# Performance work log

Hardware: AMD Instinct MI355X
Metric: run time of the kernel (lower is better)

## Reference

```python
import jax, jax.numpy as jnp
import numpy as np

V, N, H = 4, 4096, 128
EDGE_P = 0.002  # sparsity of generated adjacency


def setup_inputs() -> dict:
    key = jax.random.key(0)
    ks = jax.random.split(key, 12)
    # binary adjacency, zero diagonal (dense_to_sparse treats nonzeros as edges)
    adjs = (jax.random.uniform(ks[0], (V, N, N)) < EDGE_P).astype(jnp.float32)
    idx = jnp.arange(N)
    adjs = adjs.at[:, idx, idx].set(0.0)
    s = 0.05
    return {
        "adjs": adjs,
        "w1": jax.random.normal(ks[1], (V, N, H), jnp.float32) * s,
        "b1": jnp.zeros((V, H), jnp.float32),
        "w2": jax.random.normal(ks[2], (V, H, H), jnp.float32) * s,
        "b2": jnp.zeros((V, H), jnp.float32),
        "wa1": jax.random.normal(ks[3], (H, 64), jnp.float32) * s,
        "ba1": jnp.zeros((64,), jnp.float32),
        "wa2": jax.random.normal(ks[4], (64,), jnp.float32) * s,
        "ba2": jnp.zeros((1,), jnp.float32),
        "wf1": jax.random.normal(ks[5], (V * H, 2 * H), jnp.float32) * s,
        "bf1": jnp.zeros((2 * H,), jnp.float32),
        "wf2": jax.random.normal(ks[6], (2 * H, 128), jnp.float32) * s,
        "bf2": jnp.zeros((128,), jnp.float32),
    }


def _gcn_norm(adjs):
    # GCNConv default: A_hat = A + I, A_norm = D^-1/2 A_hat D^-1/2 (edge weight 1)
    n = adjs.shape[-1]
    idx = jnp.arange(n)
    a_hat = (adjs != 0).astype(adjs.dtype).at[:, idx, idx].set(1.0)
    dinv = jax.lax.rsqrt(a_hat.sum(-1))  # [V,N], deg>=1 due to self loops
    return dinv[:, :, None] * a_hat * dinv[:, None, :]


def reference(adjs, w1, b1, w2, b2, wa1, ba1, wa2, ba2, wf1, bf1, wf2, bf2):
    a_norm = _gcn_norm(adjs)  # [V,N,N]
    # initial features X = I_N, so X @ w1 == w1; dropout is inference no-op
    h1 = jax.nn.relu(jnp.einsum('vij,vjh->vih', a_norm, w1) + b1[:, None, :])
    h2 = jax.nn.relu(
        jnp.einsum('vij,vjh->vih', a_norm, jnp.einsum('vnh,vhk->vnk', h1, w2))
        + b2[:, None, :])  # [V,N,H] per-view embeddings
    # attention fusion
    summaries = h2.mean(axis=1)  # [V,H]
    scores = jnp.tanh(summaries @ wa1 + ba1) @ wa2 + ba2[0]  # [V]
    attn = jax.nn.softmax(scores, axis=0)  # [V]
    weighted = h2 * attn[:, None, None]  # [V,N,H]
    fusion_in = jnp.transpose(weighted, (1, 0, 2)).reshape(weighted.shape[1], -1)  # [N, V*H]
    fused = jax.nn.relu(fusion_in @ wf1 + bf1) @ wf2 + bf2  # [N, fusion_out]
    return fused, attn, h2
```

## Files before the change

kernel.cpp:

```cpp
#include <hip/hip_runtime.h>

#define VV 4
#define NN 4096
#define HH 128
#define CAP 64
#define GR 32
#define FR 8
#define CHP (NN / GR)

typedef __attribute__((ext_vector_type(4))) float fvec4;

__global__ __launch_bounds__(256) void k_build_csr(
    const float* __restrict__ adjs, int* __restrict__ nbr,
    int* __restrict__ cnt, float* __restrict__ dinv)
{
    int wave = threadIdx.x >> 6;
    int lane = threadIdx.x & 63;
    int r = blockIdx.x * 4 + wave;
    const fvec4* row = (const fvec4*)(adjs + (size_t)r * NN);
    int* out = nbr + (size_t)r * CAP;
    unsigned long long lm = (1ull << lane) - 1ull;
    int base = 0;
    #pragma unroll 4
    for (int c = 0; c < NN / 256; ++c) {
        fvec4 x = __builtin_nontemporal_load(&row[c * 64 + lane]);
        int c0 = (x.x != 0.f), c1 = (x.y != 0.f), c2 = (x.z != 0.f), c3 = (x.w != 0.f);
        unsigned long long b0 = __ballot(c0), b1 = __ballot(c1);
        unsigned long long b2 = __ballot(c2), b3 = __ballot(c3);
        int pos = base + __popcll(b0 & lm) + __popcll(b1 & lm)
                       + __popcll(b2 & lm) + __popcll(b3 & lm);
        int e = c * 256 + lane * 4;
        if (c0 && pos < CAP) out[pos] = e;     pos += c0;
        if (c1 && pos < CAP) out[pos] = e + 1; pos += c1;
        if (c2 && pos < CAP) out[pos] = e + 2; pos += c2;
        if (c3 && pos < CAP) out[pos] = e + 3; pos += c3;
        base += __popcll(b0) + __popcll(b1) + __popcll(b2) + __popcll(b3);
    }
    if (lane == 0) {
        cnt[r]  = base < CAP ? base : CAP;
        dinv[r] = rsqrtf((float)(base + 1));
    }
}

__global__ __launch_bounds__(512) void k_spmm1(
    const float* __restrict__ w1, const float* __restrict__ b1,
    const int* __restrict__ nbr, const int* __restrict__ cnt,
    const float* __restrict__ dinv, float* __restrict__ h1)
{
    int xcd  = blockIdx.x & 7;
    int slot = blockIdx.x >> 3;
    int wid  = (xcd >> 1) * 1024 + slot * 2 + (xcd & 1);
    int g = threadIdx.x >> 7;
    int h = threadIdx.x & 127;
    int r = wid * 4 + g;
    int v = r >> 12;
    __shared__ int   s_j[4][CAP];
    __shared__ float s_w[4][CAP];
    int n = cnt[r];
    float dr = dinv[r];
    if (h < n) {
        int j = nbr[(size_t)r * CAP + h];
        s_j[g][h] = j;
        s_w[g][h] = dinv[v * NN + j];
    }
    __syncthreads();
    float acc = dr * w1[(size_t)r * HH + h];
    #pragma unroll 4
    for (int k = 0; k < n; ++k)
        acc += s_w[g][k] * w1[((size_t)(v * NN + s_j[g][k])) * HH + h];
    float val = dr * acc + b1[v * HH + h];
    h1[(size_t)r * HH + h] = val > 0.f ? val : 0.f;
}

__global__ __launch_bounds__(512) void k_gather2(
    const float* __restrict__ h1, const int* __restrict__ nbr,
    const int* __restrict__ cnt, const float* __restrict__ dinv,
    float* __restrict__ u)
{
    int xcd  = blockIdx.x & 7;
    int slot = blockIdx.x >> 3;
    int wid  = (xcd >> 1) * 1024 + slot * 2 + (xcd & 1);
    int g = threadIdx.x >> 7;
    int h = threadIdx.x & 127;
    int r = wid * 4 + g;
    int v = r >> 12;
    __shared__ int   s_j[4][CAP];
    __shared__ float s_w[4][CAP];
    int n = cnt[r];
    float dr = dinv[r];
    if (h < n) {
        int j = nbr[(size_t)r * CAP + h];
        s_j[g][h] = j;
        s_w[g][h] = dinv[v * NN + j];
    }
    __syncthreads();
    float acc = dr * h1[(size_t)r * HH + h];
    #pragma unroll 4
    for (int k = 0; k < n; ++k)
        acc += s_w[g][k] * h1[((size_t)(v * NN + s_j[g][k])) * HH + h];
    u[(size_t)r * HH + h] = dr * acc;
}

__global__ __launch_bounds__(256) void k_gemm2c(
    const float* __restrict__ u, const float* __restrict__ w2,
    const float* __restrict__ b2, float* __restrict__ h2,
    float* __restrict__ part)
{
    const int bpv = NN / GR;
    int v = blockIdx.x / bpv;
    int rbase_g = blockIdx.x * GR;
    __shared__ float s_u[GR][HH];
    __shared__ float s_p[8][HH];
    const float4* src = (const float4*)(u + (size_t)rbase_g * HH);
    for (int idx = threadIdx.x; idx < GR * HH / 4; idx += 256)
        ((float4*)s_u)[idx] = src[idx];
    __syncthreads();

    int r0 = (threadIdx.x >> 5) * 4;
    int c0 = (threadIdx.x & 31) * 4;
    const float* wv = w2 + (size_t)v * HH * HH;
    float acc[4][4];
    #pragma unroll
    for (int i = 0; i < 4; ++i)
        #pragma unroll
        for (int j = 0; j < 4; ++j) acc[i][j] = 0.f;
    for (int k = 0; k < HH; k += 4) {
        float4 a[4], w[4];
        #pragma unroll
        for (int i = 0; i < 4; ++i) a[i] = *(const float4*)&s_u[r0 + i][k];
        #pragma unroll
        for (int kk = 0; kk < 4; ++kk) w[kk] = *(const float4*)&wv[(size_t)(k + kk) * HH + c0];
        #pragma unroll
        for (int i = 0; i < 4; ++i)
            #pragma unroll
            for (int j = 0; j < 4; ++j) {
                acc[i][j] += a[i].x * ((const float*)&w[0])[j];
                acc[i][j] += a[i].y * ((const float*)&w[1])[j];
                acc[i][j] += a[i].z * ((const float*)&w[2])[j];
                acc[i][j] += a[i].w * ((const float*)&w[3])[j];
            }
    }
    float p[4];
    #pragma unroll
    for (int j = 0; j < 4; ++j) {
        float b = b2[v * HH + c0 + j];
        float s = 0.f;
        #pragma unroll
        for (int i = 0; i < 4; ++i) {
            float val = acc[i][j] + b;
            val = val > 0.f ? val : 0.f;
            acc[i][j] = val;
            s += val;
        }
        p[j] = s;
    }
    float* dst = h2 + (size_t)rbase_g * HH;
    #pragma unroll
    for (int i = 0; i < 4; ++i) {
        float4 o = { acc[i][0], acc[i][1], acc[i][2], acc[i][3] };
        *(float4*)&dst[(size_t)(r0 + i) * HH + c0] = o;
    }
    *(float4*)&s_p[threadIdx.x >> 5][c0] = *(float4*)p;
    __syncthreads();
    if (threadIdx.x < HH) {
        float a = 0.f;
        #pragma unroll
        for (int q = 0; q < 8; ++q) a += s_p[q][threadIdx.x];
        part[(size_t)blockIdx.x * HH + threadIdx.x] = a;
    }
}

__global__ __launch_bounds__(512) void k_attn(
    const float* __restrict__ part, const float* __restrict__ wa1,
    const float* __restrict__ ba1, const float* __restrict__ wa2,
    const float* __restrict__ ba2, float* __restrict__ attn_out,
    float* __restrict__ attn_ws)
{
    __shared__ float s_sum[VV * HH];
    __shared__ float s_red[256];
    __shared__ float s_score[VV];
    {
        int v = threadIdx.x >> 7, h = threadIdx.x & 127;
        float a = 0.f;
        #pragma unroll 8
        for (int c = 0; c < CHP; ++c) a += part[(size_t)(v * CHP + c) * HH + h];
        s_sum[v * HH + h] = a * (1.0f / NN);
    }
    __syncthreads();
    if (threadIdx.x < 256) {
        int v = threadIdx.x >> 6, u = threadIdx.x & 63;
        float a = ba1[u];
        for (int k = 0; k < HH; ++k) a += s_sum[v * HH + k] * wa1[k * 64 + u];
        s_red[threadIdx.x] = tanhf(a) * wa2[u];
    }
    __syncthreads();
    if (threadIdx.x < VV) {
        float sc = ba2[0];
        for (int uu = 0; uu < 64; ++uu) sc += s_red[threadIdx.x * 64 + uu];
        s_score[threadIdx.x] = sc;
    }
    __syncthreads();
    if (threadIdx.x == 0) {
        float m = s_score[0];
        for (int i = 1; i < VV; ++i) m = fmaxf(m, s_score[i]);
        float e[VV], den = 0.f;
        for (int i = 0; i < VV; ++i) { e[i] = __expf(s_score[i] - m); den += e[i]; }
        for (int i = 0; i < VV; ++i) {
            float av = e[i] / den;
            attn_out[i] = av;
            attn_ws[i]  = av;
        }
    }
}

#define S1 516
#define S2 260
#define S3 132
__global__ __launch_bounds__(512) void k_fusion(
    const float* __restrict__ h2, const float* __restrict__ attn_ws,
    const float* __restrict__ wf1, const float* __restrict__ bf1,
    const float* __restrict__ wf2, const float* __restrict__ bf2,
    float* __restrict__ fused)
{
    __shared__ float s_in[FR][S1];
    __shared__ float s_hid[FR][S2];
    float (*s_part)[S2] = (float (*)[S2])&s_in[0][0];
    float (*s_p2)[S3]   = (float (*)[S3])&s_in[0][0];

    int nbase = blockIdx.x * FR;
    int wv   = threadIdx.x >> 6;
    int lane = threadIdx.x & 63;
    float at[VV];
    #pragma unroll
    for (int v = 0; v < VV; ++v) at[v] = attn_ws[v];

    for (int idx = threadIdx.x; idx < FR * 128; idx += 512) {
        int r  = idx >> 7;
        int c4 = idx & 127;
        int v  = c4 >> 5;
        int h4 = c4 & 31;
        const float4* srcr = (const float4*)(h2 + ((size_t)v * NN + nbase + r) * HH);
        float4 x = srcr[h4];
        float s = at[v];
        x.x *= s; x.y *= s; x.z *= s; x.w *= s;
        *(float4*)&s_in[r][c4 * 4] = x;
    }
    __syncthreads();

    int cg = wv & 3, kh = wv >> 2;
    int ccol  = cg * 64 + (lane & 15) * 4;
    int rbase = (lane >> 4) * 2;
    float acc[2][4];
    #pragma unroll
    for (int i = 0; i < 2; ++i)
        #pragma unroll
        for (int j = 0; j < 4; ++j) acc[i][j] = 0.f;
    {
        int k0 = kh * 256;
        const float* wrow = wf1 + (size_t)k0 * 256 + ccol;
        #pragma unroll 4
        for (int k = 0; k < 256; ++k) {
            float4 wk = *(const float4*)wrow;
            wrow += 256;
            float a0 = s_in[rbase + 0][k0 + k];
            float a1 = s_in[rbase + 1][k0 + k];
            acc[0][0] += a0 * wk.x; acc[0][1] += a0 * wk.y; acc[0][2] += a0 * wk.z; acc[0][3] += a0 * wk.w;
            acc[1][0] += a1 * wk.x; acc[1][1] += a1 * wk.y; acc[1][2] += a1 * wk.z; acc[1][3] += a1 * wk.w;
        }
    }
    __syncthreads();
    if (kh == 1) {
        #pragma unroll
        for (int i = 0; i < 2; ++i)
            *(float4*)&s_part[rbase + i][ccol] = *(float4*)&acc[i][0];
    }
    __syncthreads();
    if (kh == 0) {
        float4 b = *(const float4*)&bf1[ccol];
        #pragma unroll
        for (int i = 0; i < 2; ++i) {
            float4 p = *(float4*)&s_part[rbase + i][ccol];
            float h0  = acc[i][0] + p.x + b.x;
            float h1v = acc[i][1] + p.y + b.y;
            float h2v = acc[i][2] + p.z + b.z;
            float h3  = acc[i][3] + p.w + b.w;
            float4 o;
            o.x = h0  > 0.f ? h0  : 0.f;
            o.y = h1v > 0.f ? h1v : 0.f;
            o.z = h2v > 0.f ? h2v : 0.f;
            o.w = h3  > 0.f ? h3  : 0.f;
            *(float4*)&s_hid[rbase + i][ccol] = o;
        }
    }
    __syncthreads();

    int c2 = cg * 32 + (lane & 15) * 2;
    float acc2[2][2];
    #pragma unroll
    for (int i = 0; i < 2; ++i) { acc2[i][0] = 0.f; acc2[i][1] = 0.f; }
    {
        int k0 = kh * 128;
        const float* wrow = wf2 + (size_t)k0 * 128 + c2;
        #pragma unroll 4
        for (int k = 0; k < 128; ++k) {
            float2 wk = *(const float2*)wrow;
            wrow += 128;
            #pragma unroll
            for (int i = 0; i < 2; ++i) {
                float a = s_hid[rbase + i][k0 + k];
                acc2[i][0] += a * wk.x;
                acc2[i][1] += a * wk.y;
            }
        }
    }
    __syncthreads();
    if (kh == 1) {
        #pragma unroll
        for (int i = 0; i < 2; ++i) {
            float2 o = { acc2[i][0], acc2[i][1] };
            *(float2*)&s_p2[rbase + i][c2] = o;
        }
    }
    __syncthreads();
    if (kh == 0) {
        float b0 = bf2[c2], b1 = bf2[c2 + 1];
        #pragma unroll
        for (int i = 0; i < 2; ++i) {
            float2 p = *(float2*)&s_p2[rbase + i][c2];
            float2 o = { acc2[i][0] + p.x + b0, acc2[i][1] + p.y + b1 };
            *(float2*)&fused[(size_t)(nbase + rbase + i) * HH + c2] = o;
        }
    }
}

extern "C" void kernel_launch(void* const* d_in, const int* in_sizes, int n_in,
                              void* d_out, int out_size, void* d_ws, size_t ws_size,
                              hipStream_t stream)
{
    const float* adjs = (const float*)d_in[0];
    const float* w1   = (const float*)d_in[1];
    const float* b1   = (const float*)d_in[2];
    const float* w2   = (const float*)d_in[3];
    const float* b2   = (const float*)d_in[4];
    const float* wa1  = (const float*)d_in[5];
    const float* ba1  = (const float*)d_in[6];
    const float* wa2  = (const float*)d_in[7];
    const float* ba2  = (const float*)d_in[8];
    const float* wf1  = (const float*)d_in[9];
    const float* bf1  = (const float*)d_in[10];
    const float* wf2  = (const float*)d_in[11];
    const float* bf2  = (const float*)d_in[12];

    float* out   = (float*)d_out;
    float* fused = out;
    float* attn  = out + (size_t)NN * HH;
    float* h2    = attn + VV;

    char* w = (char*)d_ws;
    int*   nbr    = (int*)w;    w += (size_t)VV * NN * CAP * sizeof(int);
    int*   cnt    = (int*)w;    w += (size_t)VV * NN * sizeof(int);
    float* dinv   = (float*)w;  w += (size_t)VV * NN * sizeof(float);
    float* h1     = (float*)w;  w += (size_t)VV * NN * HH * sizeof(float);
    float* u      = (float*)w;  w += (size_t)VV * NN * HH * sizeof(float);
    float* part   = (float*)w;  w += (size_t)VV * CHP * HH * sizeof(float);
    float* attnws = (float*)w;  w += 256;

    k_build_csr<<<VV * NN / 4, 256, 0, stream>>>(adjs, nbr, cnt, dinv);
    k_spmm1<<<VV * NN / 4, 512, 0, stream>>>(w1, b1, nbr, cnt, dinv, h1);
    k_gather2<<<VV * NN / 4, 512, 0, stream>>>(h1, nbr, cnt, dinv, u);
    k_gemm2c<<<VV * NN / GR, 256, 0, stream>>>(u, w2, b2, h2, part);
    k_attn<<<1, 512, 0, stream>>>(part, wa1, ba1, wa2, ba2, attn, attnws);
    k_fusion<<<NN / FR, 512, 0, stream>>>(h2, attnws, wf1, bf1, wf2, bf2, fused);
}
```

Before: 151.1 us.

## Retile fusion MLP with larger row tiles and 4-way K split

The fusion kernel now processes 16 rows per block instead of 8. Each wave computes an 8-row by 4-column register tile over a quarter of the K range, and the four partial sums are reduced through shared memory. The point is to get more reuse of every wf1/wf2 weight load and to read activations as float4 from LDS, which cuts global weight traffic per output. In exchange the kernel uses more shared memory and launches half as many blocks, which can lower occupancy and parallelism.

```diff
diff --git a/kernel.cpp b/kernel.cpp
--- a/kernel.cpp
+++ b/kernel.cpp
@@ -5,8 +5,8 @@
 #define HH 128
 #define CAP 64
 #define GR 32
-#define FR 8
 #define CHP (NN / GR)
+#define FV 16
 
 typedef __attribute__((ext_vector_type(4))) float fvec4;
 
@@ -213,32 +213,29 @@
     }
 }
 
-#define S1 516
-#define S2 260
-#define S3 132
-__global__ __launch_bounds__(512) void k_fusion(
+__global__ __launch_bounds__(512) void k_fusion5(
     const float* __restrict__ h2, const float* __restrict__ attn_ws,
     const float* __restrict__ wf1, const float* __restrict__ bf1,
     const float* __restrict__ wf2, const float* __restrict__ bf2,
     float* __restrict__ fused)
 {
-    __shared__ float s_in[FR][S1];
-    __shared__ float s_hid[FR][S2];
-    float (*s_part)[S2] = (float (*)[S2])&s_in[0][0];
-    float (*s_p2)[S3]   = (float (*)[S3])&s_in[0][0];
-
-    int nbase = blockIdx.x * FR;
+    __shared__ float s_in[FV][516];
+    __shared__ float s_pt[4][FV][256];
+    __shared__ float s_hid[FV][260];
+    float (*s_p2)[FV][128] = (float (*)[FV][128])&s_pt[0][0][0];
+
+    int nbase = blockIdx.x * FV;
     int wv   = threadIdx.x >> 6;
     int lane = threadIdx.x & 63;
+    int rh = wv & 1;
+    int ks = wv >> 1;
+
     float at[VV];
     #pragma unroll
     for (int v = 0; v < VV; ++v) at[v] = attn_ws[v];
 
-    for (int idx = threadIdx.x; idx < FR * 128; idx += 512) {
-        int r  = idx >> 7;
-        int c4 = idx & 127;
-        int v  = c4 >> 5;
-        int h4 = c4 & 31;
+    for (int idx = threadIdx.x; idx < FV * 128; idx += 512) {
+        int r = idx >> 7, c4 = idx & 127, v = c4 >> 5, h4 = c4 & 31;
         const float4* srcr = (const float4*)(h2 + ((size_t)v * NN + nbase + r) * HH);
         float4 x = srcr[h4];
         float s = at[v];
@@ -247,89 +244,101 @@
     }
     __syncthreads();
 
-    int cg = wv & 3, kh = wv >> 2;
-    int ccol  = cg * 64 + (lane & 15) * 4;
-    int rbase = (lane >> 4) * 2;
-    float acc[2][4];
-    #pragma unroll
-    for (int i = 0; i < 2; ++i)
-        #pragma unroll
-        for (int j = 0; j < 4; ++j) acc[i][j] = 0.f;
-    {
-        int k0 = kh * 256;
-        const float* wrow = wf1 + (size_t)k0 * 256 + ccol;
-        #pragma unroll 4
-        for (int k = 0; k < 256; ++k) {
-            float4 wk = *(const float4*)wrow;
-            wrow += 256;
-            float a0 = s_in[rbase + 0][k0 + k];
-            float a1 = s_in[rbase + 1][k0 + k];
-            acc[0][0] += a0 * wk.x; acc[0][1] += a0 * wk.y; acc[0][2] += a0 * wk.z; acc[0][3] += a0 * wk.w;
-            acc[1][0] += a1 * wk.x; acc[1][1] += a1 * wk.y; acc[1][2] += a1 * wk.z; acc[1][3] += a1 * wk.w;
-        }
-    }
-    __syncthreads();
-    if (kh == 1) {
-        #pragma unroll
-        for (int i = 0; i < 2; ++i)
-            *(float4*)&s_part[rbase + i][ccol] = *(float4*)&acc[i][0];
-    }
-    __syncthreads();
-    if (kh == 0) {
-        float4 b = *(const float4*)&bf1[ccol];
-        #pragma unroll
-        for (int i = 0; i < 2; ++i) {
-            float4 p = *(float4*)&s_part[rbase + i][ccol];
-            float h0  = acc[i][0] + p.x + b.x;
-            float h1v = acc[i][1] + p.y + b.y;
-            float h2v = acc[i][2] + p.z + b.z;
-            float h3  = acc[i][3] + p.w + b.w;
+    {
+        int col = lane * 4;
+        int r0  = rh * 8;
+        int k0  = ks * 128;
+        float acc[8][4];
+        #pragma unroll
+        for (int i = 0; i < 8; ++i) { acc[i][0] = acc[i][1] = acc[i][2] = acc[i][3] = 0.f; }
+        const float* wrow = wf1 + (size_t)k0 * 256 + col;
+        for (int kk = 0; kk < 128; kk += 4) {
+            float4 w0 = *(const float4*)(wrow);
+            float4 w1 = *(const float4*)(wrow + 256);
+            float4 w2 = *(const float4*)(wrow + 512);
+            float4 w3 = *(const float4*)(wrow + 768);
+            wrow += 1024;
+            #pragma unroll
+            for (int i = 0; i < 8; ++i) {
+                float4 a = *(const float4*)&s_in[r0 + i][k0 + kk];
+                acc[i][0] += a.x * w0.x + a.y * w1.x + a.z * w2.x + a.w * w3.x;
+                acc[i][1] += a.x * w0.y + a.y * w1.y + a.z * w2.y + a.w * w3.y;
+                acc[i][2] += a.x * w0.z + a.y * w1.z + a.z * w2.z + a.w * w3.z;
+                acc[i][3] += a.x * w0.w + a.y * w1.w + a.z * w2.w + a.w * w3.w;
+            }
+        }
+        #pragma unroll
+        for (int i = 0; i < 8; ++i)
+            *(float4*)&s_pt[ks][r0 + i][col] = *(float4*)&acc[i][0];
+    }
+    __syncthreads();
+
+    {
+        int c0 = (threadIdx.x & 63) * 4;
+        int rr = threadIdx.x >> 6;
+        #pragma unroll
+        for (int p = 0; p < 2; ++p) {
+            int row = p * 8 + rr;
+            float4 s0 = *(float4*)&s_pt[0][row][c0];
+            float4 s1 = *(float4*)&s_pt[1][row][c0];
+            float4 s2 = *(float4*)&s_pt[2][row][c0];
+            float4 s3 = *(float4*)&s_pt[3][row][c0];
+            float4 b  = *(const float4*)&bf1[c0];
             float4 o;
-            o.x = h0  > 0.f ? h0  : 0.f;
-            o.y = h1v > 0.f ? h1v : 0.f;
-            o.z = h2v > 0.f ? h2v : 0.f;
-            o.w = h3  > 0.f ? h3  : 0.f;
-            *(float4*)&s_hid[rbase + i][ccol] = o;
-        }
-    }
-    __syncthreads();
-
-    int c2 = cg * 32 + (lane & 15) * 2;
-    float acc2[2][2];
-    #pragma unroll
-    for (int i = 0; i < 2; ++i) { acc2[i][0] = 0.f; acc2[i][1] = 0.f; }
-    {
-        int k0 = kh * 128;
-        const float* wrow = wf2 + (size_t)k0 * 128 + c2;
-        #pragma unroll 4
-        for (int k = 0; k < 128; ++k) {
-            float2 wk = *(const float2*)wrow;
-            wrow += 128;
+            o.x = s0.x + s1.x + s2.x + s3.x + b.x;
+            o.y = s0.y + s1.y + s2.y + s3.y + b.y;
+            o.z = s0.z + s1.z + s2.z + s3.z + b.z;
+            o.w = s0.w + s1.w + s2.w + s3.w + b.w;
+            o.x = o.x > 0.f ? o.x : 0.f;
+            o.y = o.y > 0.f ? o.y : 0.f;
+            o.z = o.z > 0.f ? o.z : 0.f;
+            o.w = o.w > 0.f ? o.w : 0.f;
+            *(float4*)&s_hid[row][c0] = o;
+        }
+    }
+    __syncthreads();
+
+    {
+        int col = lane * 2;
+        int r0  = rh * 8;
+        int k0  = ks * 64;
+        float acc[8][2];
+        #pragma unroll
+        for (int i = 0; i < 8; ++i) { acc[i][0] = 0.f; acc[i][1] = 0.f; }
+        const float* wrow = wf2 + (size_t)k0 * 128 + col;
+        for (int kk = 0; kk < 64; kk += 4) {
+            float2 w0 = *(const float2*)(wrow);
+            float2 w1 = *(const float2*)(wrow + 128);
+            float2 w2 = *(const float2*)(wrow + 256);
+            float2 w3 = *(const float2*)(wrow + 384);
+            wrow += 512;
             #pragma unroll
-            for (int i = 0; i < 2; ++i) {
-                float a = s_hid[rbase + i][k0 + k];
-                acc2[i][0] += a * wk.x;
-                acc2[i][1] += a * wk.y;
+            for (int i = 0; i < 8; ++i) {
+                float4 a = *(const float4*)&s_hid[r0 + i][k0 + kk];
+                acc[i][0] += a.x * w0.x + a.y * w1.x + a.z * w2.x + a.w * w3.x;
+                acc[i][1] += a.x * w0.y + a.y * w1.y + a.z * w2.y + a.w * w3.y;
             }
         }
-    }
-    __syncthreads();
-    if (kh == 1) {
-        #pragma unroll
-        for (int i = 0; i < 2; ++i) {
-            float2 o = { acc2[i][0], acc2[i][1] };
-            *(float2*)&s_p2[rbase + i][c2] = o;
-        }
-    }
-    __syncthreads();
-    if (kh == 0) {
-        float b0 = bf2[c2], b1 = bf2[c2 + 1];
-        #pragma unroll
-        for (int i = 0; i < 2; ++i) {
-            float2 p = *(float2*)&s_p2[rbase + i][c2];
-            float2 o = { acc2[i][0] + p.x + b0, acc2[i][1] + p.y + b1 };
-            *(float2*)&fused[(size_t)(nbase + rbase + i) * HH + c2] = o;
-        }
+        #pragma unroll
+        for (int i = 0; i < 8; ++i)
+            *(float2*)&s_p2[ks][r0 + i][col] = *(float2*)&acc[i][0];
+    }
+    __syncthreads();
+
+    {
+        int c0  = (threadIdx.x & 31) * 4;
+        int row = threadIdx.x >> 5;
+        float4 s0 = *(float4*)&s_p2[0][row][c0];
+        float4 s1 = *(float4*)&s_p2[1][row][c0];
+        float4 s2 = *(float4*)&s_p2[2][row][c0];
+        float4 s3 = *(float4*)&s_p2[3][row][c0];
+        float4 b  = *(const float4*)&bf2[c0];
+        float4 o;
+        o.x = s0.x + s1.x + s2.x + s3.x + b.x;
+        o.y = s0.y + s1.y + s2.y + s3.y + b.y;
+        o.z = s0.z + s1.z + s2.z + s3.z + b.z;
+        o.w = s0.w + s1.w + s2.w + s3.w + b.w;
+        *(float4*)&fused[(size_t)(nbase + row) * HH + c0] = o;
     }
 }
 
@@ -370,5 +379,5 @@
     k_gather2<<<VV * NN / 4, 512, 0, stream>>>(h1, nbr, cnt, dinv, u);
     k_gemm2c<<<VV * NN / GR, 256, 0, stream>>>(u, w2, b2, h2, part);
     k_attn<<<1, 512, 0, stream>>>(part, wa1, ba1, wa2, ba2, attn, attnws);
-    k_fusion<<<NN / FR, 512, 0, stream>>>(h2, attnws, wf1, bf1, wf2, bf2, fused);
-}
+    k_fusion5<<<NN / FV, 512, 0, stream>>>(h2, attnws, wf1, bf1, wf2, bf2, fused);
+}
```

Measured after the change: 129.3 us (median of 2 runs). 14.4% less time.
